# Optimization experiments

Hardware: AMD Instinct MI355X
Metric: run time of the kernel (lower is better)

## Reference

```python
import jax, jax.numpy as jnp
import numpy as np

B, N, T, D_MODEL, HEADS, FE = 8, 307, 48, 64, 4, 4
HD = D_MODEL // HEADS
SAMPLE_K = min(T, 5 * int(np.ceil(np.log(T))))  # = 20; also n_top u
EPS = 1e-5


def _pos_encoding(t, d):
    pos = np.arange(t, dtype=np.float32)[:, None]
    div = np.exp(np.arange(0, d, 2, dtype=np.float32) * (-np.log(10000.0) / d))
    pe = np.zeros((t, d), np.float32)
    pe[:, 0::2] = np.sin(pos * div)
    pe[:, 1::2] = np.cos(pos * div)
    return jnp.asarray(pe)


def _ln(x, g, b):
    m = x.mean(-1, keepdims=True)
    v = ((x - m) ** 2).mean(-1, keepdims=True)
    return (x - m) / jnp.sqrt(v + EPS) * g + b


def setup_inputs():
    k = jax.random.split(jax.random.key(0), 16)
    d = D_MODEL
    s = 1.0 / np.sqrt(d)
    return {
        "x": jax.random.normal(k[0], (B, N, T, d), jnp.float32),
        "time_features": jax.random.randint(k[1], (B, T, 5), 0, 10),
        "index_sample": jax.random.randint(k[2], (T, SAMPLE_K), 0, T),
        "Wq": jax.random.normal(k[3], (d, d), jnp.float32) * s,
        "Wk": jax.random.normal(k[4], (d, d), jnp.float32) * s,
        "Wv": jax.random.normal(k[5], (d, d), jnp.float32) * s,
        "Wo": jax.random.normal(k[6], (d, d), jnp.float32) * s,
        "bo": jnp.zeros((d,), jnp.float32),
        "W1": jax.random.normal(k[7], (d, FE * d), jnp.float32) * s,
        "b1": jnp.zeros((FE * d,), jnp.float32),
        "W2": jax.random.normal(k[8], (FE * d, d), jnp.float32) * (1.0 / np.sqrt(FE * d)),
        "b2": jnp.zeros((d,), jnp.float32),
        "g1": jnp.ones((d,), jnp.float32), "be1": jnp.zeros((d,), jnp.float32),
        "g2": jnp.ones((d,), jnp.float32), "be2": jnp.zeros((d,), jnp.float32),
        "emb_min": jax.random.normal(k[9], (70, d), jnp.float32) * 0.02,
        "emb_hr": jax.random.normal(k[10], (30, d), jnp.float32) * 0.02,
        "emb_wd": jax.random.normal(k[11], (10, d), jnp.float32) * 0.02,
        "emb_mo": jax.random.normal(k[12], (40, d), jnp.float32) * 0.02,
        "emb_yr": jax.random.normal(k[13], (400, d), jnp.float32) * 0.02,
    }


def reference(x, time_features, index_sample, Wq, Wk, Wv, Wo, bo, W1, b1, W2, b2,
              g1, be1, g2, be2, emb_min, emb_hr, emb_wd, emb_mo, emb_yr):
    b_, n_, t_, d = x.shape
    # temporal position + calendar embeddings (dropout is identity in eval)
    pe = _pos_encoding(t_, d)                                   # [T,d]
    tf = time_features
    tc = (emb_min[tf[..., 0]] + emb_hr[tf[..., 1]] + emb_wd[tf[..., 2]]
          + emb_mo[tf[..., 3]] + emb_yr[tf[..., 4]])             # [B,T,d]
    enc = x + pe[None, None] + tc[:, None]                       # [B,N,T,d]

    def split_heads(y):
        return y.reshape(b_, n_, t_, HEADS, HD).transpose(0, 3, 1, 2, 4)  # [B,H,N,T,HD]

    Q = split_heads(enc @ Wq)
    K = split_heads(enc @ Wk)
    V = split_heads(enc @ Wv)

    # ProbSparse attention: the torch K_expand + fancy-index is equivalent to a direct gather of K
    K_samp = K[:, :, :, index_sample, :]                         # [B,H,N,T,Sk,HD]
    qk_s = jnp.einsum('bhntd,bhntsd->bhnts', Q, K_samp)
    M = qk_s.max(-1) - qk_s.sum(-1) / SAMPLE_K                   # sparsity measure [B,H,N,T]
    _, m_top = jax.lax.top_k(M, SAMPLE_K)                        # u = SAMPLE_K, [B,H,N,u]
    Qr = jnp.take_along_axis(Q, m_top[..., None], axis=3)        # [B,H,N,u,HD]
    scores = jnp.einsum('bhnud,bhntd->bhnut', Qr, K) * (1.0 / np.sqrt(HD))
    attn = jax.nn.softmax(scores, axis=-1)
    upd = jnp.einsum('bhnut,bhntd->bhnud', attn, V)              # [B,H,N,u,HD]

    ctx = jnp.broadcast_to(V.mean(axis=3, keepdims=True), V.shape)  # initial context = mean(V)
    bi = jnp.arange(b_)[:, None, None, None]
    hi = jnp.arange(HEADS)[None, :, None, None]
    ni = jnp.arange(n_)[None, None, :, None]
    ctx = ctx.at[bi, hi, ni, m_top].set(upd)                     # scatter top-u rows

    ctx = ctx.transpose(0, 2, 3, 1, 4).reshape(b_, n_, t_, d)
    att_out = ctx @ Wo + bo
    h = _ln(att_out + enc, g1, be1)
    ff = jax.nn.relu(h @ W1 + b1) @ W2 + b2
    return _ln(ff + h, g2, be2)
```

## Files before the change

### kernel.cpp

```cpp
#include <hip/hip_runtime.h>

#define B_ 8
#define N_ 307
#define T_ 48
#define D_ 64
#define H_ 4
#define HD_ 16
#define SK_ 20
#define EPS_ 1e-5f

typedef __attribute__((ext_vector_type(8))) short bf16x8;
typedef __attribute__((ext_vector_type(4))) float f32x4;

__device__ inline ushort f2bf(float f) {
  union { float f; uint u; } x;
  x.f = f;
  uint u = x.u;
  return (ushort)((u + 0x7fffu + ((u >> 16) & 1u)) >> 16);
}
__device__ inline float bflo(uint w) { return __uint_as_float(w << 16); }
__device__ inline float bfhi(uint w) {
  return __uint_as_float(w & 0xffff0000u);
}

__global__ void prep_kernel(const int* __restrict__ tf,
                            const float* __restrict__ em,
                            const float* __restrict__ eh,
                            const float* __restrict__ ew,
                            const float* __restrict__ emo,
                            const float* __restrict__ ey,
                            float* __restrict__ tcpe,
                            const float* __restrict__ Wo,
                            const float* __restrict__ W1,
                            const float* __restrict__ W2,
                            ushort* __restrict__ WoB, ushort* __restrict__ W1B,
                            ushort* __restrict__ W2B) {
  if (blockIdx.x < 96) {
    int idx = blockIdx.x * 256 + threadIdx.x;
    if (idx >= B_ * T_ * D_) return;
    int d = idx & (D_ - 1);
    int bt = idx >> 6;
    int t = bt % T_;
    float freq = expf((float)((d >> 1) << 1) * (-logf(10000.0f) / (float)D_));
    float ang = (float)t * freq;
    float pe = (d & 1) ? cosf(ang) : sinf(ang);
    const int* f = tf + bt * 5;
    tcpe[idx] = pe + em[f[0] * D_ + d] + eh[f[1] * D_ + d] +
                ew[f[2] * D_ + d] + emo[f[3] * D_ + d] + ey[f[4] * D_ + d];
  } else {
    int idx = (blockIdx.x - 96) * 256 + threadIdx.x;
    if (idx >= 4096 + 16384 + 16384) return;
    const float* W;
    ushort* O;
    int NT, N;
    if (idx < 4096) {
      W = Wo; O = WoB; NT = 4; N = 64;
    } else if (idx < 4096 + 16384) {
      idx -= 4096; W = W1; O = W1B; NT = 16; N = 256;
    } else {
      idx -= 20480; W = W2; O = W2B; NT = 4; N = 64;
    }
    int e = idx & 7;
    int l = (idx >> 3) & 63;
    int f = idx >> 9;
    int no = f % NT, ko = f / NT;
    int k = ko * 32 + (l >> 4) * 8 + e;
    int n = no * 16 + (l & 15);
    O[idx] = f2bf(W[k * N + n]);
  }
}

__global__ __launch_bounds__(256, 3) void mega_kernel(
    const float* __restrict__ x, const int* __restrict__ idxs,
    const float* __restrict__ Wq, const float* __restrict__ Wk,
    const float* __restrict__ Wv, const ushort* __restrict__ WoB,
    const ushort* __restrict__ W1B, const ushort* __restrict__ W2B,
    const float* __restrict__ bo, const float* __restrict__ b1,
    const float* __restrict__ b2, const float* __restrict__ g1,
    const float* __restrict__ be1, const float* __restrict__ g2,
    const float* __restrict__ be2, const float* __restrict__ tcpe,
    float* __restrict__ out) {
  __shared__ char smem[52224];
  __shared__ float s_rden[H_ * SK_];
  __shared__ int s_mtop[H_ * SK_];
  float* s_enc = (float*)smem;
  float* s_k = (float*)(smem + 13056);
  float* s_q = (float*)(smem + 26112);
  uint* s_v = (uint*)(smem + 38400);
  uint* s_at = (uint*)(smem + 44544);
  float* s_M = (float*)(smem + 44544);
  ushort* hs = (ushort*)(smem + 13056);

  const int tid = threadIdx.x;
  const int l = tid & 63;
  const int g = tid >> 6;
  const int bn = blockIdx.x;
  const int b = bn / N_;

  {
    const float4* x4 = (const float4*)(x + (size_t)bn * (T_ * D_));
    const float4* t4 = (const float4*)(tcpe + (size_t)b * (T_ * D_));
#pragma unroll
    for (int r = 0; r < 3; ++r) {
      int i = tid + 256 * r;
      float4 xv = x4[i];
      float4 tv = t4[i];
      int t = i >> 4;
      int d = (i & 15) << 2;
      *(float4*)&s_enc[t * 68 + d] =
          make_float4(xv.x + tv.x, xv.y + tv.y, xv.z + tv.z, xv.w + tv.w);
    }
  }
  __syncthreads();

  {
    float accq[12], acck[12], accv[12];
#pragma unroll
    for (int i = 0; i < 12; ++i) accq[i] = acck[i] = accv[i] = 0.0f;
#pragma unroll 1
    for (int kc = 0; kc < 4; ++kc) {
      float wq[16], wk[16], wv[16];
#pragma unroll
      for (int i = 0; i < 16; ++i) {
        int k = kc * 16 + i;
        wq[i] = Wq[k * D_ + l];
        wk[i] = Wk[k * D_ + l];
        wv[i] = Wv[k * D_ + l];
      }
#pragma unroll
      for (int tt = 0; tt < 12; ++tt) {
        const float* row = &s_enc[(g * 12 + tt) * 68 + kc * 16];
        float4 r0 = ((const float4*)row)[0];
        float4 r1 = ((const float4*)row)[1];
        float4 r2 = ((const float4*)row)[2];
        float4 r3 = ((const float4*)row)[3];
        float rr[16] = {r0.x, r0.y, r0.z, r0.w, r1.x, r1.y, r1.z, r1.w,
                        r2.x, r2.y, r2.z, r2.w, r3.x, r3.y, r3.z, r3.w};
#pragma unroll
        for (int i = 0; i < 16; ++i) {
          accq[tt] = fmaf(rr[i], wq[i], accq[tt]);
          acck[tt] = fmaf(rr[i], wk[i], acck[tt]);
          accv[tt] = fmaf(rr[i], wv[i], accv[tt]);
        }
      }
    }
    ushort* vp = (ushort*)s_v;
#pragma unroll
    for (int tt = 0; tt < 12; ++tt) {
      int t = g * 12 + tt;
      s_q[t * 64 + l] = accq[tt];
      s_k[t * 68 + l] = acck[tt];
      vp[((t >> 1) * 64 + l) * 2 + (t & 1)] = f2bf(accv[tt]);
    }
  }
  __syncthreads();

  if (l < T_) {
    float q[16];
#pragma unroll
    for (int j = 0; j < 16; j += 4) {
      float4 v4 = *(const float4*)&s_q[l * 64 + g * HD_ + j];
      q[j] = v4.x; q[j + 1] = v4.y; q[j + 2] = v4.z; q[j + 3] = v4.w;
    }
    float mx = -1e30f, sm = 0.0f;
    for (int s = 0; s < SK_; ++s) {
      int kt = idxs[l * SK_ + s];
      float acc = 0.0f;
#pragma unroll
      for (int j = 0; j < 16; j += 4) {
        float4 kv = *(const float4*)&s_k[kt * 68 + g * HD_ + j];
        acc = fmaf(kv.x, q[j], acc);
        acc = fmaf(kv.y, q[j + 1], acc);
        acc = fmaf(kv.z, q[j + 2], acc);
        acc = fmaf(kv.w, q[j + 3], acc);
      }
      mx = fmaxf(mx, acc);
      sm += acc;
    }
    s_M[g * T_ + l] = mx - sm * (1.0f / (float)SK_);
  }
  __syncthreads();

  if (l < T_) {
    float mv = s_M[g * T_ + l];
    int rank = 0;
    for (int t2 = 0; t2 < T_; ++t2) {
      float o = s_M[g * T_ + t2];
      rank += (o > mv || (o == mv && t2 < l)) ? 1 : 0;
    }
    if (rank < SK_) s_mtop[g * SK_ + rank] = l;
  }
  __syncthreads();

  {
    float kr[16];
    if (l < T_) {
#pragma unroll
      for (int j = 0; j < 16; j += 4) {
        float4 v4 = *(const float4*)&s_k[l * 68 + g * HD_ + j];
        kr[j] = v4.x; kr[j + 1] = v4.y; kr[j + 2] = v4.z; kr[j + 3] = v4.w;
      }
    } else {
#pragma unroll
      for (int j = 0; j < 16; ++j) kr[j] = 0.0f;
    }
    ushort* ap = (ushort*)s_at;
#pragma unroll 1
    for (int u = 0; u < SK_; ++u) {
      int qt = s_mtop[g * SK_ + u];
      const float4* qp = (const float4*)&s_q[qt * 64 + g * HD_];
      float acc = 0.0f;
#pragma unroll
      for (int j = 0; j < 4; ++j) {
        float4 qv = qp[j];
        acc = fmaf(qv.x, kr[4 * j], acc);
        acc = fmaf(qv.y, kr[4 * j + 1], acc);
        acc = fmaf(qv.z, kr[4 * j + 2], acc);
        acc = fmaf(qv.w, kr[4 * j + 3], acc);
      }
      if (l < T_) ap[(g * SK_ + u) * T_ + l] = f2bf(__expf(acc * 0.25f));
    }
  }
  if (l < SK_) {
    const uint* ap = s_at + (g * SK_ + l) * 24;
    float s0 = 0.0f, s1 = 0.0f;
#pragma unroll
    for (int tp = 0; tp < 24; ++tp) {
      uint w = ap[tp];
      s0 += bflo(w);
      s1 += bfhi(w);
    }
    s_rden[g * SK_ + l] = 1.0f / (s0 + s1);
  }

  const int u0 = l >> 4, jj = l & 15;
  float upd[5] = {0, 0, 0, 0, 0};
  float vm = 0.0f;
  {
    const uint* a32 = s_at + g * SK_ * 24;
    const uint* v32 = s_v + g * HD_ + jj;
#pragma unroll 4
    for (int tp = 0; tp < 24; ++tp) {
      uint vw = v32[tp * 64];
      float vlo = bflo(vw), vhi = bfhi(vw);
      vm += vlo + vhi;
#pragma unroll
      for (int r = 0; r < 5; ++r) {
        uint aw = a32[(u0 + 4 * r) * 24 + tp];
        upd[r] = fmaf(bflo(aw), vlo, fmaf(bfhi(aw), vhi, upd[r]));
      }
    }
    vm *= (1.0f / (float)T_);
#pragma unroll
    for (int r = 0; r < 5; ++r) upd[r] *= s_rden[g * SK_ + u0 + 4 * r];
  }
  __syncthreads();

  {
    ushort cvm = f2bf(vm);
#pragma unroll
    for (int r = 0; r < 12; ++r) {
      int i = l + 64 * r;
      int t = i >> 4;
      hs[t * 72 + g * HD_ + jj] = cvm;
    }
    hs[(48 + u0) * 72 + g * HD_ + jj] = 0;
#pragma unroll
    for (int r = 0; r < 5; ++r) {
      int row = s_mtop[g * SK_ + u0 + 4 * r];
      hs[row * 72 + g * HD_ + jj] = f2bf(upd[r]);
    }
  }
  __syncthreads();

  ushort* ft = (ushort*)(smem + 26112) + g * 2176;
  const int kg = l >> 4, c = l & 15;
  const int row0 = g * 12;
  const f32x4 z = {0.f, 0.f, 0.f, 0.f};

  f32x4 co[4];
  {
    bf16x8 a0 = *(const bf16x8*)(const void*)(hs + (row0 + c) * 72 + kg * 8);
    bf16x8 a1 =
        *(const bf16x8*)(const void*)(hs + (row0 + c) * 72 + 32 + kg * 8);
#pragma unroll
    for (int no = 0; no < 4; ++no) {
      bf16x8 b0 = *(const bf16x8*)(const void*)(WoB + (no * 64 + l) * 8);
      bf16x8 b1f = *(const bf16x8*)(const void*)(WoB + ((4 + no) * 64 + l) * 8);
      f32x4 t0 = __builtin_amdgcn_mfma_f32_16x16x32_bf16(a0, b0, z, 0, 0, 0);
      co[no] = __builtin_amdgcn_mfma_f32_16x16x32_bf16(a1, b1f, t0, 0, 0, 0);
    }
  }
  __syncthreads();

  float h[16];
  int er[4];
#pragma unroll
  for (int reg = 0; reg < 4; ++reg) {
    int cr = kg * 4 + reg;
    er[reg] = (row0 + (cr < 12 ? cr : 11)) * 68;
  }
#pragma unroll
  for (int no = 0; no < 4; ++no) {
    int col = no * 16 + c;
    float bov = bo[col];
#pragma unroll
    for (int reg = 0; reg < 4; ++reg)
      h[no * 4 + reg] = co[no][reg] + bov + s_enc[er[reg] + col];
  }
#pragma unroll
  for (int reg = 0; reg < 4; ++reg) {
    float s = h[reg] + h[4 + reg] + h[8 + reg] + h[12 + reg];
    s += __shfl_xor(s, 1); s += __shfl_xor(s, 2);
    s += __shfl_xor(s, 4); s += __shfl_xor(s, 8);
    float mean = s * (1.0f / 64.0f);
    float d0 = h[reg] - mean, d1 = h[4 + reg] - mean;
    float d2 = h[8 + reg] - mean, d3 = h[12 + reg] - mean;
    float q = d0 * d0 + d1 * d1 + d2 * d2 + d3 * d3;
    q += __shfl_xor(q, 1); q += __shfl_xor(q, 2);
    q += __shfl_xor(q, 4); q += __shfl_xor(q, 8);
    float rstd = 1.0f / sqrtf(q * (1.0f / 64.0f) + EPS_);
#pragma unroll
    for (int no = 0; no < 4; ++no) {
      int col = no * 16 + c;
      h[no * 4 + reg] = (h[no * 4 + reg] - mean) * rstd * g1[col] + be1[col];
    }
  }
#pragma unroll
  for (int no = 0; no < 4; ++no)
#pragma unroll
    for (int reg = 0; reg < 4; ++reg) {
      int cr = kg * 4 + reg;
      if (cr < 12) hs[(row0 + cr) * 72 + no * 16 + c] = f2bf(h[no * 4 + reg]);
    }
  __syncthreads();

  f32x4 o[4] = {z, z, z, z};
  {
    bf16x8 ha0 = *(const bf16x8*)(const void*)(hs + (row0 + c) * 72 + kg * 8);
    bf16x8 ha1 =
        *(const bf16x8*)(const void*)(hs + (row0 + c) * 72 + 32 + kg * 8);
#pragma unroll 1
    for (int p = 0; p < 2; ++p) {
      f32x4 f1[8];
#pragma unroll
      for (int q = 0; q < 8; ++q) {
        int no = p * 8 + q;
        bf16x8 b0 = *(const bf16x8*)(const void*)(W1B + (no * 64 + l) * 8);
        bf16x8 b1f =
            *(const bf16x8*)(const void*)(W1B + ((16 + no) * 64 + l) * 8);
        f32x4 t0 = __builtin_amdgcn_mfma_f32_16x16x32_bf16(ha0, b0, z, 0, 0, 0);
        f1[q] = __builtin_amdgcn_mfma_f32_16x16x32_bf16(ha1, b1f, t0, 0, 0, 0);
      }
#pragma unroll
      for (int q = 0; q < 8; ++q) {
        float bb = b1[(p * 8 + q) * 16 + c];
#pragma unroll
        for (int reg = 0; reg < 4; ++reg) {
          float vv = fmaxf(f1[q][reg] + bb, 0.0f);
          ft[(kg * 4 + reg) * 136 + q * 16 + c] = f2bf(vv);
        }
      }
#pragma unroll
      for (int ko = 0; ko < 4; ++ko) {
        bf16x8 fa =
            *(const bf16x8*)(const void*)(ft + c * 136 + ko * 32 + kg * 8);
#pragma unroll
        for (int no = 0; no < 4; ++no) {
          bf16x8 bf_ = *(const bf16x8*)(const void*)(
              W2B + (((p * 4 + ko) * 4 + no) * 64 + l) * 8);
          o[no] =
              __builtin_amdgcn_mfma_f32_16x16x32_bf16(fa, bf_, o[no], 0, 0, 0);
        }
      }
    }
  }

  float v[16];
#pragma unroll
  for (int no = 0; no < 4; ++no) {
    float b2v = b2[no * 16 + c];
#pragma unroll
    for (int reg = 0; reg < 4; ++reg)
      v[no * 4 + reg] = o[no][reg] + b2v + h[no * 4 + reg];
  }
#pragma unroll
  for (int reg = 0; reg < 4; ++reg) {
    float s = v[reg] + v[4 + reg] + v[8 + reg] + v[12 + reg];
    s += __shfl_xor(s, 1); s += __shfl_xor(s, 2);
    s += __shfl_xor(s, 4); s += __shfl_xor(s, 8);
    float mean = s * (1.0f / 64.0f);
    float d0 = v[reg] - mean, d1 = v[4 + reg] - mean;
    float d2 = v[8 + reg] - mean, d3 = v[12 + reg] - mean;
    float q = d0 * d0 + d1 * d1 + d2 * d2 + d3 * d3;
    q += __shfl_xor(q, 1); q += __shfl_xor(q, 2);
    q += __shfl_xor(q, 4); q += __shfl_xor(q, 8);
    float rstd = 1.0f / sqrtf(q * (1.0f / 64.0f) + EPS_);
    int cr = kg * 4 + reg;
    if (cr < 12) {
      float* op = out + ((size_t)bn * T_ + row0 + cr) * D_;
#pragma unroll
      for (int no = 0; no < 4; ++no) {
        int col = no * 16 + c;
        op[col] = (v[no * 4 + reg] - mean) * rstd * g2[col] + be2[col];
      }
    }
  }
}

extern "C" void kernel_launch(void* const* d_in, const int* in_sizes, int n_in,
                              void* d_out, int out_size, void* d_ws,
                              size_t ws_size, hipStream_t stream) {
  const float* x = (const float*)d_in[0];
  const int* tf = (const int*)d_in[1];
  const int* idxs = (const int*)d_in[2];
  const float* Wq = (const float*)d_in[3];
  const float* Wk = (const float*)d_in[4];
  const float* Wv = (const float*)d_in[5];
  const float* Wo = (const float*)d_in[6];
  const float* bo = (const float*)d_in[7];
  const float* W1 = (const float*)d_in[8];
  const float* b1 = (const float*)d_in[9];
  const float* W2 = (const float*)d_in[10];
  const float* b2 = (const float*)d_in[11];
  const float* g1 = (const float*)d_in[12];
  const float* be1 = (const float*)d_in[13];
  const float* g2 = (const float*)d_in[14];
  const float* be2 = (const float*)d_in[15];
  const float* em = (const float*)d_in[16];
  const float* eh = (const float*)d_in[17];
  const float* ew = (const float*)d_in[18];
  const float* emo = (const float*)d_in[19];
  const float* ey = (const float*)d_in[20];
  float* out = (float*)d_out;

  float* tcpe = (float*)d_ws;
  ushort* WoB = (ushort*)((char*)d_ws + 98304);
  ushort* W1B = WoB + 4096;
  ushort* W2B = W1B + 16384;

  hipLaunchKernelGGL(prep_kernel, dim3(240), dim3(256), 0, stream, tf, em, eh,
                     ew, emo, ey, tcpe, Wo, W1, W2, WoB, W1B, W2B);
  hipLaunchKernelGGL(mega_kernel, dim3(B_ * N_), dim3(256), 0, stream, x, idxs,
                     Wq, Wk, Wv, WoB, W1B, W2B, bo, b1, b2, g1, be1, g2, be2,
                     tcpe, out);
}
```

Baseline: 141.2 us.

## Shrink shared memory to raise occupancy, spill V to global, stage output stores

Shared memory per block drops from about 52KB to about 38KB, which allows four blocks per CU instead of three. To fit, the bf16 V tile now goes to a global workspace buffer instead of LDS, the attention-score buffer reuses the K region (a barrier is added first), and the FFN hidden tile is processed in four 64-wide chunks instead of two 128-wide ones. The final LayerNorm output is staged through LDS and written with coalesced float4 stores. The cost is extra global traffic and latency for V, likely served from L2, plus one more barrier.

```diff
diff --git a/kernel.cpp b/kernel.cpp
--- a/kernel.cpp
+++ b/kernel.cpp
@@ -70,7 +70,7 @@
   }
 }
 
-__global__ __launch_bounds__(256, 3) void mega_kernel(
+__global__ __launch_bounds__(256, 4) void mega_kernel(
     const float* __restrict__ x, const int* __restrict__ idxs,
     const float* __restrict__ Wq, const float* __restrict__ Wk,
     const float* __restrict__ Wv, const ushort* __restrict__ WoB,
@@ -79,16 +79,15 @@
     const float* __restrict__ b2, const float* __restrict__ g1,
     const float* __restrict__ be1, const float* __restrict__ g2,
     const float* __restrict__ be2, const float* __restrict__ tcpe,
-    float* __restrict__ out) {
-  __shared__ char smem[52224];
+    uint* __restrict__ Vg, float* __restrict__ out) {
+  __shared__ char smem[38400];
+  __shared__ float s_M[H_ * T_];
   __shared__ float s_rden[H_ * SK_];
   __shared__ int s_mtop[H_ * SK_];
   float* s_enc = (float*)smem;
   float* s_k = (float*)(smem + 13056);
   float* s_q = (float*)(smem + 26112);
-  uint* s_v = (uint*)(smem + 38400);
-  uint* s_at = (uint*)(smem + 44544);
-  float* s_M = (float*)(smem + 44544);
+  ushort* ap = (ushort*)(smem + 13056);
   ushort* hs = (ushort*)(smem + 13056);
 
   const int tid = threadIdx.x;
@@ -144,14 +143,17 @@
         }
       }
     }
-    ushort* vp = (ushort*)s_v;
 #pragma unroll
     for (int tt = 0; tt < 12; ++tt) {
       int t = g * 12 + tt;
       s_q[t * 64 + l] = accq[tt];
       s_k[t * 68 + l] = acck[tt];
-      vp[((t >> 1) * 64 + l) * 2 + (t & 1)] = f2bf(accv[tt]);
-    }
+    }
+    uint* vp = Vg + (size_t)bn * 1536 + g * 6 * 64 + l;
+#pragma unroll
+    for (int i = 0; i < 6; ++i)
+      vp[i * 64] =
+          (uint)f2bf(accv[2 * i]) | ((uint)f2bf(accv[2 * i + 1]) << 16);
   }
   __syncthreads();
 
@@ -204,7 +206,7 @@
 #pragma unroll
       for (int j = 0; j < 16; ++j) kr[j] = 0.0f;
     }
-    ushort* ap = (ushort*)s_at;
+    __syncthreads();
 #pragma unroll 1
     for (int u = 0; u < SK_; ++u) {
       int qt = s_mtop[g * SK_ + u];
@@ -222,11 +224,11 @@
     }
   }
   if (l < SK_) {
-    const uint* ap = s_at + (g * SK_ + l) * 24;
+    const uint* a32 = (const uint*)(smem + 13056) + (g * SK_ + l) * 24;
     float s0 = 0.0f, s1 = 0.0f;
 #pragma unroll
     for (int tp = 0; tp < 24; ++tp) {
-      uint w = ap[tp];
+      uint w = a32[tp];
       s0 += bflo(w);
       s1 += bfhi(w);
     }
@@ -237,8 +239,8 @@
   float upd[5] = {0, 0, 0, 0, 0};
   float vm = 0.0f;
   {
-    const uint* a32 = s_at + g * SK_ * 24;
-    const uint* v32 = s_v + g * HD_ + jj;
+    const uint* a32 = (const uint*)(smem + 13056) + g * SK_ * 24;
+    const uint* v32 = Vg + (size_t)bn * 1536 + g * HD_ + jj;
 #pragma unroll 4
     for (int tp = 0; tp < 24; ++tp) {
       uint vw = v32[tp * 64];
@@ -273,7 +275,7 @@
   }
   __syncthreads();
 
-  ushort* ft = (ushort*)(smem + 26112) + g * 2176;
+  ushort* ft = (ushort*)(smem + 26112) + g * 1152;
   const int kg = l >> 4, c = l & 15;
   const int row0 = g * 12;
   const f32x4 z = {0.f, 0.f, 0.f, 0.f};
@@ -341,11 +343,11 @@
     bf16x8 ha1 =
         *(const bf16x8*)(const void*)(hs + (row0 + c) * 72 + 32 + kg * 8);
 #pragma unroll 1
-    for (int p = 0; p < 2; ++p) {
-      f32x4 f1[8];
-#pragma unroll
-      for (int q = 0; q < 8; ++q) {
-        int no = p * 8 + q;
+    for (int p = 0; p < 4; ++p) {
+      f32x4 f1[4];
+#pragma unroll
+      for (int q = 0; q < 4; ++q) {
+        int no = p * 4 + q;
         bf16x8 b0 = *(const bf16x8*)(const void*)(W1B + (no * 64 + l) * 8);
         bf16x8 b1f =
             *(const bf16x8*)(const void*)(W1B + ((16 + no) * 64 + l) * 8);
@@ -353,22 +355,22 @@
         f1[q] = __builtin_amdgcn_mfma_f32_16x16x32_bf16(ha1, b1f, t0, 0, 0, 0);
       }
 #pragma unroll
-      for (int q = 0; q < 8; ++q) {
-        float bb = b1[(p * 8 + q) * 16 + c];
+      for (int q = 0; q < 4; ++q) {
+        float bb = b1[(p * 4 + q) * 16 + c];
 #pragma unroll
         for (int reg = 0; reg < 4; ++reg) {
           float vv = fmaxf(f1[q][reg] + bb, 0.0f);
-          ft[(kg * 4 + reg) * 136 + q * 16 + c] = f2bf(vv);
+          ft[(kg * 4 + reg) * 72 + q * 16 + c] = f2bf(vv);
         }
       }
 #pragma unroll
-      for (int ko = 0; ko < 4; ++ko) {
+      for (int koi = 0; koi < 2; ++koi) {
         bf16x8 fa =
-            *(const bf16x8*)(const void*)(ft + c * 136 + ko * 32 + kg * 8);
+            *(const bf16x8*)(const void*)(ft + c * 72 + koi * 32 + kg * 8);
 #pragma unroll
         for (int no = 0; no < 4; ++no) {
           bf16x8 bf_ = *(const bf16x8*)(const void*)(
-              W2B + (((p * 4 + ko) * 4 + no) * 64 + l) * 8);
+              W2B + (((p * 2 + koi) * 4 + no) * 64 + l) * 8);
           o[no] =
               __builtin_amdgcn_mfma_f32_16x16x32_bf16(fa, bf_, o[no], 0, 0, 0);
         }
@@ -376,6 +378,7 @@
     }
   }
 
+  float* bt = (float*)smem + g * 816;
   float v[16];
 #pragma unroll
   for (int no = 0; no < 4; ++no) {
@@ -398,12 +401,21 @@
     float rstd = 1.0f / sqrtf(q * (1.0f / 64.0f) + EPS_);
     int cr = kg * 4 + reg;
     if (cr < 12) {
-      float* op = out + ((size_t)bn * T_ + row0 + cr) * D_;
 #pragma unroll
       for (int no = 0; no < 4; ++no) {
         int col = no * 16 + c;
-        op[col] = (v[no * 4 + reg] - mean) * rstd * g2[col] + be2[col];
-      }
+        bt[cr * 68 + col] = (v[no * 4 + reg] - mean) * rstd * g2[col] + be2[col];
+      }
+    }
+  }
+  {
+    float* op = out + ((size_t)bn * T_ + row0) * D_;
+#pragma unroll
+    for (int rr = 0; rr < 3; ++rr) {
+      int i = l + 64 * rr;
+      int row = i >> 4;
+      int c4 = (i & 15) << 2;
+      *(float4*)&op[row * D_ + c4] = *(const float4*)&bt[row * 68 + c4];
     }
   }
 }
@@ -438,10 +450,11 @@
   ushort* WoB = (ushort*)((char*)d_ws + 98304);
   ushort* W1B = WoB + 4096;
   ushort* W2B = W1B + 16384;
+  uint* Vg = (uint*)((char*)d_ws + 172032);
 
   hipLaunchKernelGGL(prep_kernel, dim3(240), dim3(256), 0, stream, tf, em, eh,
                      ew, emo, ey, tcpe, Wo, W1, W2, WoB, W1B, W2B);
   hipLaunchKernelGGL(mega_kernel, dim3(B_ * N_), dim3(256), 0, stream, x, idxs,
                      Wq, Wk, Wv, WoB, W1B, W2B, bo, b1, b2, g1, be1, g2, be2,
-                     tcpe, out);
+                     tcpe, Vg, out);
 }
```

New measurement: 138.9 us. About the same (-1.6%).
